# Kernel tuning notes

Hardware: AMD Instinct MI355X
Metric: run time of the kernel (lower is better)

The kernel has to match this reference:

```python
import jax, jax.numpy as jnp
import numpy as np

B, T, F, H = 256, 1024, 64, 128
DT = 1.0
EPS = 1e-5


def _layer_norm(h, g, b):
    mu = jnp.mean(h, axis=-1, keepdims=True)
    var = jnp.var(h, axis=-1, keepdims=True)
    return (h - mu) * jax.lax.rsqrt(var + EPS) * g + b


def setup_inputs() -> dict:
    key = jax.random.key(0)
    ks = jax.random.split(key, 8)
    def xavier(k, shape):
        fan_in, fan_out = shape[1], shape[0]
        lim = np.sqrt(6.0 / (fan_in + fan_out))
        return jax.random.uniform(k, shape, jnp.float32, -lim, lim)
    return {
        "x": jax.random.normal(ks[0], (B, T, F), jnp.float32),
        # layer 0 (input_dim=F)
        "Wh0": xavier(ks[1], (H, H)), "bh0": jnp.zeros((H,), jnp.float32),
        "Wx0": xavier(ks[2], (H, F)), "bx0": jnp.zeros((H,), jnp.float32),
        "Wt0": xavier(ks[3], (H, F)), "bt0": jnp.zeros((H,), jnp.float32),
        "tau0": jnp.ones((H,), jnp.float32),
        "g0": jnp.ones((H,), jnp.float32), "be0": jnp.zeros((H,), jnp.float32),
        # layer 1 (input_dim=H)
        "Wh1": xavier(ks[4], (H, H)), "bh1": jnp.zeros((H,), jnp.float32),
        "Wx1": xavier(ks[5], (H, H)), "bx1": jnp.zeros((H,), jnp.float32),
        "Wt1": xavier(ks[6], (H, H)), "bt1": jnp.zeros((H,), jnp.float32),
        "tau1": jnp.ones((H,), jnp.float32),
        "g1": jnp.ones((H,), jnp.float32), "be1": jnp.zeros((H,), jnp.float32),
    }


def _cell(x_t, h, Wh, bh, Wx, bx, Wt, bt, tau_base):
    f = jnp.tanh(h @ Wh.T + bh + x_t @ Wx.T + bx)        # (B,H)
    tau = tau_base + jax.nn.softplus(x_t @ Wt.T + bt)     # (B,H)
    return h + (DT / tau) * (-h + f)


def reference(x, Wh0, bh0, Wx0, bx0, Wt0, bt0, tau0, g0, be0,
              Wh1, bh1, Wx1, bx1, Wt1, bt1, tau1, g1, be1):
    xT = jnp.transpose(x, (1, 0, 2))  # (T,B,F)

    def step(carry, x_t):
        h0, h1 = carry
        h0 = _layer_norm(_cell(x_t, h0, Wh0, bh0, Wx0, bx0, Wt0, bt0, tau0), g0, be0)
        h1 = _layer_norm(_cell(h0, h1, Wh1, bh1, Wx1, bx1, Wt1, bt1, tau1), g1, be1)
        return (h0, h1), None

    h_init = (jnp.zeros((x.shape[0], H), x.dtype), jnp.zeros((x.shape[0], H), x.dtype))
    (h0, h1), _ = jax.lax.scan(step, h_init, xT)
    return h1  # hidden_dim == latent_dim, no proj
```

## Files before the change

kernel.cpp:

```cpp
#include <hip/hip_runtime.h>
#include <stdint.h>


#define B_ 256
#define T_ 1024
#define F_ 64
#define H_ 128
#define EPS_ 1e-5f
#define NT_ 512

typedef _Float16 h2 __attribute__((ext_vector_type(2)));
typedef _Float16 h8 __attribute__((ext_vector_type(8)));
typedef float f32x4 __attribute__((ext_vector_type(4)));
typedef __fp16  f16v2 __attribute__((ext_vector_type(2)));

__device__ __forceinline__ h2 pkf16(float a, float b) {
  union { f16v2 f; h2 h; } c;
  c.f = __builtin_amdgcn_cvt_pkrtz(a, b);
  return c.h;
}
__device__ __forceinline__ uint32_t as_u32(h2 h) { union { h2 h; uint32_t u; } c; c.h = h; return c.u; }

#if __has_builtin(__builtin_amdgcn_rsqf)
__device__ __forceinline__ float rsq_fast(float x) { return __builtin_amdgcn_rsqf(x); }
#else
__device__ __forceinline__ float rsq_fast(float x) { return rsqrtf(x); }
#endif

#if __has_builtin(__builtin_amdgcn_update_dpp)
template <int CTRL>
__device__ __forceinline__ float dpp_add(float v) {
  union { float f; int i; } a, b;
  a.f = v;
  b.i = __builtin_amdgcn_update_dpp(0, a.i, CTRL, 0xf, 0xf, true);
  return v + b.f;
}
__device__ __forceinline__ float red16(float v) {
  v = dpp_add<0x128>(v);
  v = dpp_add<0x124>(v);
  v = dpp_add<0x122>(v);
  v = dpp_add<0x121>(v);
  return v;
}
#else
__device__ __forceinline__ float red16(float v) {
  v += __shfl_xor(v, 1); v += __shfl_xor(v, 2);
  v += __shfl_xor(v, 4); v += __shfl_xor(v, 8);
  return v;
}
#endif

__device__ __forceinline__ h8 packfrag(const float* p) {
  float4 a = *(const float4*)p;
  float4 b = *(const float4*)(p + 4);
  union { h2 h[4]; h8 v; } c;
  c.h[0] = pkf16(a.x, a.y); c.h[1] = pkf16(a.z, a.w);
  c.h[2] = pkf16(b.x, b.y); c.h[3] = pkf16(b.z, b.w);
  return c.v;
}
__device__ __forceinline__ h8 packfrag_g(const float* w, const float* gv, const float* bv,
                                         float& dg, float& dbe) {
  float4 a = *(const float4*)w;
  float4 b = *(const float4*)(w + 4);
  float4 ga = *(const float4*)gv;
  float4 gb = *(const float4*)(gv + 4);
  float4 ba = *(const float4*)bv;
  float4 bb = *(const float4*)(bv + 4);
  float w0 = a.x*ga.x, w1 = a.y*ga.y, w2 = a.z*ga.z, w3 = a.w*ga.w;
  float w4 = b.x*gb.x, w5 = b.y*gb.y, w6 = b.z*gb.z, w7 = b.w*gb.w;
  dg  += (w0 + w1) + (w2 + w3) + (w4 + w5) + (w6 + w7);
  dbe += a.x*ba.x + a.y*ba.y + a.z*ba.z + a.w*ba.w
       + b.x*bb.x + b.y*bb.y + b.z*bb.z + b.w*bb.w;
  union { h2 h[4]; h8 v; } c;
  c.h[0] = pkf16(w0, w1); c.h[1] = pkf16(w2, w3);
  c.h[2] = pkf16(w4, w5); c.h[3] = pkf16(w6, w7);
  return c.v;
}
__device__ __forceinline__ h8 ldfrag(const uint32_t* p) {
  union { uint4 u; h8 v; } c;
  c.u = *(const uint4*)p;
  return c.v;
}

__device__ __forceinline__ float tanh_fast(float a) {
  float aa = fabsf(a);
  float e  = __expf(2.f * aa);
  float th = 1.f - 2.f * __builtin_amdgcn_rcpf(e + 1.f);
  return copysignf(th, a);
}
__device__ __forceinline__ float softplus_fast(float x) {
  return (x > 20.f) ? x : __logf(1.f + __expf(x));
}

#define MFMA16(A_, B_, C_) __builtin_amdgcn_mfma_f32_16x16x32_f16(A_, B_, C_, 0, 0, 0)

__global__ void __attribute__((amdgpu_flat_work_group_size(NT_, NT_)))
                __attribute__((amdgpu_waves_per_eu(2, 2)))
ltc_scan(
    const float* __restrict__ x,
    const float* __restrict__ Wh0, const float* __restrict__ bh0,
    const float* __restrict__ Wx0, const float* __restrict__ bx0,
    const float* __restrict__ Wt0, const float* __restrict__ bt0,
    const float* __restrict__ tau0, const float* __restrict__ g0,
    const float* __restrict__ be0,
    const float* __restrict__ Wh1, const float* __restrict__ bh1,
    const float* __restrict__ Wx1, const float* __restrict__ bx1,
    const float* __restrict__ Wt1, const float* __restrict__ bt1,
    const float* __restrict__ tau1, const float* __restrict__ g1,
    const float* __restrict__ be1,
    float* __restrict__ out)
{
  __shared__ __align__(16) uint32_t h0p[2][64];
  __shared__ __align__(16) uint32_t h1p[2][64];
  __shared__ __align__(16) uint32_t x4[4][32];
  __shared__ __align__(16) float    part[4][4];

  const int tid = threadIdx.x;
  const int wid = tid >> 6;
  const int l   = tid & 63;
  const int g4  = (l >> 4) << 2;
  const int g8  = (l >> 4) << 3;
  const int b   = blockIdx.x;
  const float* xg = x + (size_t)b * (T_ * F_);
  const bool selT1 = (l & 16) != 0;

  if (tid < 128) { ((uint32_t*)h0p)[tid] = 0u; ((uint32_t*)h1p)[tid] = 0u; }
  if (tid < 16)  ((float*)part)[tid] = 0.f;
  if (tid < 32) {
    float2 a = *(const float2*)(xg + 2 * tid);
    float2 c = *(const float2*)(xg + F_ + 2 * tid);
    x4[0][tid] = as_u32(pkf16(a.x, a.y));
    x4[1][tid] = as_u32(pkf16(c.x, c.y));
  }
  __syncthreads();

  if (wid < 4) {
    const int c0 = wid * 32 + (l & 15);
    const int ct = wid * 32 + (l & 31);
    h8 wh0[4], wh1[4], wx0[2], wx1[2], wt0[2], wt1[2];
    float cg, cb;
    {
      float dg0 = 0.f, db0 = 0.f, dg1 = 0.f, db1 = 0.f;
      const float* p0 = Wh0 + c0 * H_ + g8;
      const float* p1 = Wh0 + (c0 + 16) * H_ + g8;
      #pragma unroll
      for (int m = 0; m < 4; ++m) {
        wh0[m] = packfrag_g(p0 + 32 * m, g0 + g8 + 32 * m, be0 + g8 + 32 * m, dg0, db0);
        wh1[m] = packfrag_g(p1 + 32 * m, g0 + g8 + 32 * m, be0 + g8 + 32 * m, dg1, db1);
      }
      dg0 += __shfl_xor(dg0, 16); dg0 += __shfl_xor(dg0, 32);
      db0 += __shfl_xor(db0, 16); db0 += __shfl_xor(db0, 32);
      dg1 += __shfl_xor(dg1, 16); dg1 += __shfl_xor(dg1, 32);
      db1 += __shfl_xor(db1, 16); db1 += __shfl_xor(db1, 32);
      cg = selT1 ? dg1 : dg0; cb = selT1 ? db1 : db0;
      const float* q0 = Wx0 + c0 * F_ + g8;
      const float* q1 = Wx0 + (c0 + 16) * F_ + g8;
      const float* r0 = Wt0 + c0 * F_ + g8;
      const float* r1 = Wt0 + (c0 + 16) * F_ + g8;
      #pragma unroll
      for (int m = 0; m < 2; ++m) {
        wx0[m] = packfrag(q0 + 32 * m); wx1[m] = packfrag(q1 + 32 * m);
        wt0[m] = packfrag(r0 + 32 * m); wt1[m] = packfrag(r1 + 32 * m);
      }
    }
    const float bhx = bh0[ct] + bx0[ct];
    const float btr = bt0[ct], taub = tau0[ct], gr = g0[ct], ber = be0[ct];
    const int  widx = wid * 16 + ((l & 31) >> 1);
    const bool wlane = ((l & 33) == 0);
    const bool st = (wid == 0) && (l < 32);

    float hcp = 0.f;
    float2 xcur;
    if (st) xcur = *(const float2*)(xg + 2 * F_ + 2 * l);

    #pragma unroll 4
    for (int i = 0; i <= T_; ++i) {
      const float2 stt = *(const float2*)&part[(i + 3) & 3][0];
      if (st) {
        x4[(i + 2) & 3][l] = as_u32(pkf16(xcur.x, xcur.y));
        int tn = (i + 3 < T_) ? (i + 3) : (T_ - 1);
        xcur = *(const float2*)(xg + tn * F_ + 2 * l);
      }
      const uint32_t* ub = h0p[(i + 1) & 1];
      const uint32_t* xb = x4[i & 3];
      f32x4 aH0 = {0.f,0.f,0.f,0.f}, aH1 = {0.f,0.f,0.f,0.f};
      f32x4 aX0 = {0.f,0.f,0.f,0.f}, aX1 = {0.f,0.f,0.f,0.f};
      f32x4 aT0 = {0.f,0.f,0.f,0.f}, aT1 = {0.f,0.f,0.f,0.f};
      #pragma unroll
      for (int m = 0; m < 4; ++m) {
        h8 af = ldfrag(ub + m * 16 + g4);
        aH0 = MFMA16(af, wh0[m], aH0);
        aH1 = MFMA16(af, wh1[m], aH1);
      }
      #pragma unroll
      for (int m = 0; m < 2; ++m) {
        h8 xf = ldfrag(xb + m * 16 + g4);
        aX0 = MFMA16(xf, wx0[m], aX0);
        aX1 = MFMA16(xf, wx1[m], aX1);
        aT0 = MFMA16(xf, wt0[m], aT0);
        aT1 = MFMA16(xf, wt1[m], aT1);
      }
      float aH = selT1 ? aH1[0] : aH0[0];
      float aX = selT1 ? aX1[0] : aX0[0];
      float aT = selT1 ? aT1[0] : aT0[0];
      float mu = stt.x * (1.f / 128.f);
      float m2 = stt.y * (1.f / 128.f);
      float rstd = rsq_fast(m2 - mu * mu + EPS_);
      float fl = (i > 0) ? 1.f : 0.f;
      float sc = fl * rstd;
      float pa = fmaf(sc, aH, fmaf(-sc * mu, cg, fl * cb)) + aX + bhx;
      float pt = aT + btr;
      float f   = tanh_fast(pa);
      float tau = taub + softplus_fast(pt);
      float hold = fl * fmaf((hcp - mu) * rstd, gr, ber);
      float hc  = fmaf(f - hold, __builtin_amdgcn_rcpf(tau), hold);
      float hc2 = __shfl_xor(hc, 1);
      if (wlane) h0p[i & 1][widx] = as_u32(pkf16(hc, hc2));
      float v = (l & 32) ? hc * hc : hc;
      v = red16(v); v += __shfl_xor(v, 16);
      if (l == 0)  atomicAdd(&part[i & 3][0], v);
      if (l == 32) atomicAdd(&part[i & 3][1], v);
      hcp = hc;
      __syncthreads();
    }
  } else {
    const int c0 = (wid - 4) * 32 + (l & 15);
    const int ct = (wid - 4) * 32 + (l & 31);
    h8 vh0[4], vh1[4], vx0[4], vx1[4], vt0[4], vt1[4];
    float cAg, cAb, cBg, cBb, cTg, cTb;
    {
      float d1=0.f,d2=0.f,d3=0.f,d4=0.f,d5=0.f,d6=0.f;
      float e1=0.f,e2=0.f,e3=0.f,e4=0.f,e5=0.f,e6=0.f;
      const float* p0 = Wh1 + c0 * H_ + g8;
      const float* p1 = Wh1 + (c0 + 16) * H_ + g8;
      const float* q0 = Wx1 + c0 * H_ + g8;
      const float* q1 = Wx1 + (c0 + 16) * H_ + g8;
      const float* r0 = Wt1 + c0 * H_ + g8;
      const float* r1 = Wt1 + (c0 + 16) * H_ + g8;
      #pragma unroll
      for (int m = 0; m < 4; ++m) {
        vh0[m] = packfrag_g(p0 + 32 * m, g1 + g8 + 32 * m, be1 + g8 + 32 * m, d1, d2);
        vh1[m] = packfrag_g(p1 + 32 * m, g1 + g8 + 32 * m, be1 + g8 + 32 * m, e1, e2);
        vx0[m] = packfrag_g(q0 + 32 * m, g0 + g8 + 32 * m, be0 + g8 + 32 * m, d3, d4);
        vx1[m] = packfrag_g(q1 + 32 * m, g0 + g8 + 32 * m, be0 + g8 + 32 * m, e3, e4);
        vt0[m] = packfrag_g(r0 + 32 * m, g0 + g8 + 32 * m, be0 + g8 + 32 * m, d5, d6);
        vt1[m] = packfrag_g(r1 + 32 * m, g0 + g8 + 32 * m, be0 + g8 + 32 * m, e5, e6);
      }
      d1 += __shfl_xor(d1, 16); d1 += __shfl_xor(d1, 32);
      d2 += __shfl_xor(d2, 16); d2 += __shfl_xor(d2, 32);
      d3 += __shfl_xor(d3, 16); d3 += __shfl_xor(d3, 32);
      d4 += __shfl_xor(d4, 16); d4 += __shfl_xor(d4, 32);
      d5 += __shfl_xor(d5, 16); d5 += __shfl_xor(d5, 32);
      d6 += __shfl_xor(d6, 16); d6 += __shfl_xor(d6, 32);
      e1 += __shfl_xor(e1, 16); e1 += __shfl_xor(e1, 32);
      e2 += __shfl_xor(e2, 16); e2 += __shfl_xor(e2, 32);
      e3 += __shfl_xor(e3, 16); e3 += __shfl_xor(e3, 32);
      e4 += __shfl_xor(e4, 16); e4 += __shfl_xor(e4, 32);
      e5 += __shfl_xor(e5, 16); e5 += __shfl_xor(e5, 32);
      e6 += __shfl_xor(e6, 16); e6 += __shfl_xor(e6, 32);
      cAg = selT1 ? e1 : d1; cAb = selT1 ? e2 : d2;
      cBg = selT1 ? e3 : d3; cBb = selT1 ? e4 : d4;
      cTg = selT1 ? e5 : d5; cTb = selT1 ? e6 : d6;
    }
    const float bhx = bh1[ct] + bx1[ct];
    const float btr = bt1[ct], taub = tau1[ct], gr = g1[ct], ber = be1[ct];
    const int  widx = (wid - 4) * 16 + ((l & 31) >> 1);
    const bool wlane = ((l & 33) == 0);
    const bool zt = (tid == NT_ - 1);

    float hcp = 0.f;
    #pragma unroll 2
    for (int i = 0; i <= T_; ++i) {
      const float4 P = *(const float4*)&part[(i + 3) & 3][0];
      if (zt) *(float4*)&part[(i + 2) & 3][0] = make_float4(0.f, 0.f, 0.f, 0.f);
      const uint32_t* u1b = h1p[(i + 1) & 1];
      const uint32_t* u0b = h0p[(i + 1) & 1];
      f32x4 aA0 = {0.f,0.f,0.f,0.f}, aA1 = {0.f,0.f,0.f,0.f};
      f32x4 aB0 = {0.f,0.f,0.f,0.f}, aB1 = {0.f,0.f,0.f,0.f};
      f32x4 aT0 = {0.f,0.f,0.f,0.f}, aT1 = {0.f,0.f,0.f,0.f};
      #pragma unroll
      for (int m = 0; m < 4; ++m) {
        h8 af = ldfrag(u1b + m * 16 + g4);
        aA0 = MFMA16(af, vh0[m], aA0);
        aA1 = MFMA16(af, vh1[m], aA1);
      }
      #pragma unroll
      for (int m = 0; m < 4; ++m) {
        h8 f0 = ldfrag(u0b + m * 16 + g4);
        aB0 = MFMA16(f0, vx0[m], aB0);
        aB1 = MFMA16(f0, vx1[m], aB1);
        aT0 = MFMA16(f0, vt0[m], aT0);
        aT1 = MFMA16(f0, vt1[m], aT1);
      }
      float aA = selT1 ? aA1[0] : aA0[0];
      float aB = selT1 ? aB1[0] : aB0[0];
      float aT = selT1 ? aT1[0] : aT0[0];
      float mu0 = P.x * (1.f / 128.f), m20 = P.y * (1.f / 128.f);
      float mu1 = P.z * (1.f / 128.f), m21 = P.w * (1.f / 128.f);
      float rstd0 = rsq_fast(m20 - mu0 * mu0 + EPS_);
      float rstd1 = rsq_fast(m21 - mu1 * mu1 + EPS_);
      float fl0 = (i > 0) ? 1.f : 0.f;
      float fl1 = (i > 1) ? 1.f : 0.f;
      float sc0 = fl0 * rstd0, sc1 = fl1 * rstd1;
      float pa = fmaf(sc1, aA, fmaf(-sc1 * mu1, cAg, fl1 * cAb))
               + fmaf(sc0, aB, fmaf(-sc0 * mu0, cBg, fl0 * cBb)) + bhx;
      float pt = fmaf(sc0, aT, fmaf(-sc0 * mu0, cTg, fl0 * cTb)) + btr;
      float f   = tanh_fast(pa);
      float tau = taub + softplus_fast(pt);
      float hold = fl1 * fmaf((hcp - mu1) * rstd1, gr, ber);
      float hc  = fmaf(f - hold, __builtin_amdgcn_rcpf(tau), hold);
      float hc2 = __shfl_xor(hc, 1);
      bool we = (i > 0);
      if (we && wlane) h1p[i & 1][widx] = as_u32(pkf16(hc, hc2));
      float v = (l & 32) ? hc * hc : hc;
      v = red16(v); v += __shfl_xor(v, 16);
      if (we && l == 0)  atomicAdd(&part[i & 3][2], v);
      if (we && l == 32) atomicAdd(&part[i & 3][3], v);
      if (we) hcp = hc;
      __syncthreads();
    }
    {
      float mu1 = part[T_ & 3][2] * (1.f / 128.f);
      float m21 = part[T_ & 3][3] * (1.f / 128.f);
      float rstd1 = rsq_fast(m21 - mu1 * mu1 + EPS_);
      float hn = fmaf((hcp - mu1) * rstd1, gr, ber);
      if (l < 32) out[b * H_ + ct] = hn;
    }
  }
}

extern "C" void kernel_launch(void* const* d_in, const int* in_sizes, int n_in,
                              void* d_out, int out_size, void* d_ws, size_t ws_size,
                              hipStream_t stream) {
  const float* x    = (const float*)d_in[0];
  const float* Wh0  = (const float*)d_in[1];
  const float* bh0  = (const float*)d_in[2];
  const float* Wx0  = (const float*)d_in[3];
  const float* bx0  = (const float*)d_in[4];
  const float* Wt0  = (const float*)d_in[5];
  const float* bt0  = (const float*)d_in[6];
  const float* tau0 = (const float*)d_in[7];
  const float* g0   = (const float*)d_in[8];
  const float* be0  = (const float*)d_in[9];
  const float* Wh1  = (const float*)d_in[10];
  const float* bh1  = (const float*)d_in[11];
  const float* Wx1  = (const float*)d_in[12];
  const float* bx1  = (const float*)d_in[13];
  const float* Wt1  = (const float*)d_in[14];
  const float* bt1  = (const float*)d_in[15];
  const float* tau1 = (const float*)d_in[16];
  const float* g1   = (const float*)d_in[17];
  const float* be1  = (const float*)d_in[18];
  float* out        = (float*)d_out;

  ltc_scan<<<B_, NT_, 0, stream>>>(x, Wh0, bh0, Wx0, bx0, Wt0, bt0, tau0, g0, be0,
                                   Wh1, bh1, Wx1, bx1, Wt1, bt1, tau1, g1, be1, out);
}
```

Before: 1.015 ms.

## Pack two batch rows per 1024-thread block to halve block count

Each block now handles two independent batch rows with 16 waves, using per-row shared buffers and statistics slots, and the grid is halved. The aim is to raise per-CU occupancy and overlap two independent recurrences so each one's latency is hidden. The cost is that only half as many blocks run, both rows share one barrier per step, and the tighter waves-per-EU bound cuts the register budget, which may force weight fragments to spill.

```diff
diff --git a/kernel.cpp b/kernel.cpp
--- a/kernel.cpp
+++ b/kernel.cpp
@@ -7,7 +7,7 @@
 #define F_ 64
 #define H_ 128
 #define EPS_ 1e-5f
-#define NT_ 512
+#define NT_ 1024
 
 typedef _Float16 h2 __attribute__((ext_vector_type(2)));
 typedef _Float16 h8 __attribute__((ext_vector_type(8)));
@@ -95,7 +95,7 @@
 #define MFMA16(A_, B_, C_) __builtin_amdgcn_mfma_f32_16x16x32_f16(A_, B_, C_, 0, 0, 0)
 
 __global__ void __attribute__((amdgpu_flat_work_group_size(NT_, NT_)))
-                __attribute__((amdgpu_waves_per_eu(2, 2)))
+                __attribute__((amdgpu_waves_per_eu(4, 4)))
 ltc_scan(
     const float* __restrict__ x,
     const float* __restrict__ Wh0, const float* __restrict__ bh0,
@@ -110,33 +110,35 @@
     const float* __restrict__ be1,
     float* __restrict__ out)
 {
-  __shared__ __align__(16) uint32_t h0p[2][64];
-  __shared__ __align__(16) uint32_t h1p[2][64];
-  __shared__ __align__(16) uint32_t x4[4][32];
-  __shared__ __align__(16) float    part[4][4];
+  __shared__ __align__(16) uint32_t h0p[2][2][64];
+  __shared__ __align__(16) uint32_t h1p[2][2][64];
+  __shared__ __align__(16) uint32_t x4[2][4][32];
+  __shared__ __align__(16) float    part[2][4][4];
 
   const int tid = threadIdx.x;
   const int wid = tid >> 6;
+  const int r   = wid >> 3;
+  const int w8  = wid & 7;
   const int l   = tid & 63;
   const int g4  = (l >> 4) << 2;
   const int g8  = (l >> 4) << 3;
-  const int b   = blockIdx.x;
-  const float* xg = x + (size_t)b * (T_ * F_);
+  const int row = blockIdx.x * 2 + r;
+  const float* xg = x + (size_t)row * (T_ * F_);
   const bool selT1 = (l & 16) != 0;
 
-  if (tid < 128) { ((uint32_t*)h0p)[tid] = 0u; ((uint32_t*)h1p)[tid] = 0u; }
-  if (tid < 16)  ((float*)part)[tid] = 0.f;
-  if (tid < 32) {
-    float2 a = *(const float2*)(xg + 2 * tid);
-    float2 c = *(const float2*)(xg + F_ + 2 * tid);
-    x4[0][tid] = as_u32(pkf16(a.x, a.y));
-    x4[1][tid] = as_u32(pkf16(c.x, c.y));
+  if (tid < 256) { ((uint32_t*)h0p)[tid] = 0u; ((uint32_t*)h1p)[tid] = 0u; }
+  if (tid < 32)  ((float*)part)[tid] = 0.f;
+  if (w8 == 0 && l < 32) {
+    float2 a = *(const float2*)(xg + 2 * l);
+    float2 c = *(const float2*)(xg + F_ + 2 * l);
+    x4[r][0][l] = as_u32(pkf16(a.x, a.y));
+    x4[r][1][l] = as_u32(pkf16(c.x, c.y));
   }
   __syncthreads();
 
-  if (wid < 4) {
-    const int c0 = wid * 32 + (l & 15);
-    const int ct = wid * 32 + (l & 31);
+  if (w8 < 4) {
+    const int c0 = w8 * 32 + (l & 15);
+    const int ct = w8 * 32 + (l & 31);
     h8 wh0[4], wh1[4], wx0[2], wx1[2], wt0[2], wt1[2];
     float cg, cb;
     {
@@ -165,9 +167,9 @@
     }
     const float bhx = bh0[ct] + bx0[ct];
     const float btr = bt0[ct], taub = tau0[ct], gr = g0[ct], ber = be0[ct];
-    const int  widx = wid * 16 + ((l & 31) >> 1);
+    const int  widx = w8 * 16 + ((l & 31) >> 1);
     const bool wlane = ((l & 33) == 0);
-    const bool st = (wid == 0) && (l < 32);
+    const bool st = (w8 == 0) && (l < 32);
 
     float hcp = 0.f;
     float2 xcur;
@@ -175,14 +177,14 @@
 
     #pragma unroll 4
     for (int i = 0; i <= T_; ++i) {
-      const float2 stt = *(const float2*)&part[(i + 3) & 3][0];
+      const float2 stt = *(const float2*)&part[r][(i + 3) & 3][0];
       if (st) {
-        x4[(i + 2) & 3][l] = as_u32(pkf16(xcur.x, xcur.y));
+        x4[r][(i + 2) & 3][l] = as_u32(pkf16(xcur.x, xcur.y));
         int tn = (i + 3 < T_) ? (i + 3) : (T_ - 1);
         xcur = *(const float2*)(xg + tn * F_ + 2 * l);
       }
-      const uint32_t* ub = h0p[(i + 1) & 1];
-      const uint32_t* xb = x4[i & 3];
+      const uint32_t* ub = h0p[r][(i + 1) & 1];
+      const uint32_t* xb = x4[r][i & 3];
       f32x4 aH0 = {0.f,0.f,0.f,0.f}, aH1 = {0.f,0.f,0.f,0.f};
       f32x4 aX0 = {0.f,0.f,0.f,0.f}, aX1 = {0.f,0.f,0.f,0.f};
       f32x4 aT0 = {0.f,0.f,0.f,0.f}, aT1 = {0.f,0.f,0.f,0.f};
@@ -215,17 +217,17 @@
       float hold = fl * fmaf((hcp - mu) * rstd, gr, ber);
       float hc  = fmaf(f - hold, __builtin_amdgcn_rcpf(tau), hold);
       float hc2 = __shfl_xor(hc, 1);
-      if (wlane) h0p[i & 1][widx] = as_u32(pkf16(hc, hc2));
+      if (wlane) h0p[r][i & 1][widx] = as_u32(pkf16(hc, hc2));
       float v = (l & 32) ? hc * hc : hc;
       v = red16(v); v += __shfl_xor(v, 16);
-      if (l == 0)  atomicAdd(&part[i & 3][0], v);
-      if (l == 32) atomicAdd(&part[i & 3][1], v);
+      if (l == 0)  atomicAdd(&part[r][i & 3][0], v);
+      if (l == 32) atomicAdd(&part[r][i & 3][1], v);
       hcp = hc;
       __syncthreads();
     }
   } else {
-    const int c0 = (wid - 4) * 32 + (l & 15);
-    const int ct = (wid - 4) * 32 + (l & 31);
+    const int c0 = (w8 - 4) * 32 + (l & 15);
+    const int ct = (w8 - 4) * 32 + (l & 31);
     h8 vh0[4], vh1[4], vx0[4], vx1[4], vt0[4], vt1[4];
     float cAg, cAb, cBg, cBb, cTg, cTb;
     {
@@ -264,17 +266,17 @@
     }
     const float bhx = bh1[ct] + bx1[ct];
     const float btr = bt1[ct], taub = tau1[ct], gr = g1[ct], ber = be1[ct];
-    const int  widx = (wid - 4) * 16 + ((l & 31) >> 1);
+    const int  widx = (w8 - 4) * 16 + ((l & 31) >> 1);
     const bool wlane = ((l & 33) == 0);
-    const bool zt = (tid == NT_ - 1);
+    const bool zt = (w8 == 7 && l == 63);
 
     float hcp = 0.f;
     #pragma unroll 2
     for (int i = 0; i <= T_; ++i) {
-      const float4 P = *(const float4*)&part[(i + 3) & 3][0];
-      if (zt) *(float4*)&part[(i + 2) & 3][0] = make_float4(0.f, 0.f, 0.f, 0.f);
-      const uint32_t* u1b = h1p[(i + 1) & 1];
-      const uint32_t* u0b = h0p[(i + 1) & 1];
+      const float4 P = *(const float4*)&part[r][(i + 3) & 3][0];
+      if (zt) *(float4*)&part[r][(i + 2) & 3][0] = make_float4(0.f, 0.f, 0.f, 0.f);
+      const uint32_t* u1b = h1p[r][(i + 1) & 1];
+      const uint32_t* u0b = h0p[r][(i + 1) & 1];
       f32x4 aA0 = {0.f,0.f,0.f,0.f}, aA1 = {0.f,0.f,0.f,0.f};
       f32x4 aB0 = {0.f,0.f,0.f,0.f}, aB1 = {0.f,0.f,0.f,0.f};
       f32x4 aT0 = {0.f,0.f,0.f,0.f}, aT1 = {0.f,0.f,0.f,0.f};
@@ -311,20 +313,20 @@
       float hc  = fmaf(f - hold, __builtin_amdgcn_rcpf(tau), hold);
       float hc2 = __shfl_xor(hc, 1);
       bool we = (i > 0);
-      if (we && wlane) h1p[i & 1][widx] = as_u32(pkf16(hc, hc2));
+      if (we && wlane) h1p[r][i & 1][widx] = as_u32(pkf16(hc, hc2));
       float v = (l & 32) ? hc * hc : hc;
       v = red16(v); v += __shfl_xor(v, 16);
-      if (we && l == 0)  atomicAdd(&part[i & 3][2], v);
-      if (we && l == 32) atomicAdd(&part[i & 3][3], v);
+      if (we && l == 0)  atomicAdd(&part[r][i & 3][2], v);
+      if (we && l == 32) atomicAdd(&part[r][i & 3][3], v);
       if (we) hcp = hc;
       __syncthreads();
     }
     {
-      float mu1 = part[T_ & 3][2] * (1.f / 128.f);
-      float m21 = part[T_ & 3][3] * (1.f / 128.f);
+      float mu1 = part[r][T_ & 3][2] * (1.f / 128.f);
+      float m21 = part[r][T_ & 3][3] * (1.f / 128.f);
       float rstd1 = rsq_fast(m21 - mu1 * mu1 + EPS_);
       float hn = fmaf((hcp - mu1) * rstd1, gr, ber);
-      if (l < 32) out[b * H_ + ct] = hn;
+      if (l < 32) out[row * H_ + ct] = hn;
     }
   }
 }
@@ -353,6 +355,6 @@
   const float* be1  = (const float*)d_in[18];
   float* out        = (float*)d_out;
 
-  ltc_scan<<<B_, NT_, 0, stream>>>(x, Wh0, bh0, Wx0, bx0, Wt0, bt0, tau0, g0, be0,
-                                   Wh1, bh1, Wx1, bx1, Wt1, bt1, tau1, g1, be1, out);
-}
+  ltc_scan<<<B_ / 2, NT_, 0, stream>>>(x, Wh0, bh0, Wx0, bx0, Wt0, bt0, tau0, g0, be0,
+                                       Wh1, bh1, Wx1, bx1, Wt1, bt1, tau1, g1, be1, out);
+}
```

Measured after the change: 2.730 ms. 2.69x slower.

## Replace per-step block barriers with LDS flag-based producer/consumer sync between layer waves

Applied to the files above, without the earlier changes.

Replaces the __syncthreads at every timestep with per-wave done counters in shared memory that are polled with s_sleep. Layer-0 waves can now run up to three steps ahead of layer-1 waves through 4-deep ring buffers for hidden states and partial sums. The LDS atomicAdd reductions become per-wave partial-sum slots that consumers add up, and the layer-1 loop is re-indexed so its one-step skew no longer needs an extra iteration. The intent is to decouple the two layers and remove lock-step barrier stalls. The cost is spin-wait polling overhead and reliance on volatile LDS ordering being correct.

```diff
diff --git a/kernel.cpp b/kernel.cpp
--- a/kernel.cpp
+++ b/kernel.cpp
@@ -49,6 +49,17 @@
   return v;
 }
 #endif
+
+__device__ __forceinline__ void wait4(volatile int* a, int tgt) {
+  if (tgt <= 0) return;
+  for (;;) {
+    int m0 = a[0], m1 = a[1], m2 = a[2], m3 = a[3];
+    int m = min(min(m0, m1), min(m2, m3));
+    if (m >= tgt) break;
+    __builtin_amdgcn_s_sleep(1);
+  }
+  __threadfence_block();
+}
 
 __device__ __forceinline__ h8 packfrag(const float* p) {
   float4 a = *(const float4*)p;
@@ -110,10 +121,13 @@
     const float* __restrict__ be1,
     float* __restrict__ out)
 {
-  __shared__ __align__(16) uint32_t h0p[2][64];
-  __shared__ __align__(16) uint32_t h1p[2][64];
-  __shared__ __align__(16) uint32_t x4[4][32];
-  __shared__ __align__(16) float    part[4][4];
+  __shared__ __align__(16) uint32_t h0p[4][64];
+  __shared__ __align__(16) uint32_t h1p[4][64];
+  __shared__ __align__(16) uint32_t x4r[4][32];
+  __shared__ __align__(16) float2   p0s[4][4];
+  __shared__ __align__(16) float2   p1s[4][4];
+  __shared__ volatile int done0[4];
+  __shared__ volatile int done1[4];
 
   const int tid = threadIdx.x;
   const int wid = tid >> 6;
@@ -124,13 +138,14 @@
   const float* xg = x + (size_t)b * (T_ * F_);
   const bool selT1 = (l & 16) != 0;
 
-  if (tid < 128) { ((uint32_t*)h0p)[tid] = 0u; ((uint32_t*)h1p)[tid] = 0u; }
-  if (tid < 16)  ((float*)part)[tid] = 0.f;
+  if (tid < 256) { ((uint32_t*)h0p)[tid] = 0u; ((uint32_t*)h1p)[tid] = 0u; }
+  if (tid < 32)  { ((float*)p0s)[tid] = 0.f; ((float*)p1s)[tid] = 0.f; }
+  if (tid < 4)   { done0[tid] = 0; done1[tid] = 0; }
   if (tid < 32) {
     float2 a = *(const float2*)(xg + 2 * tid);
     float2 c = *(const float2*)(xg + F_ + 2 * tid);
-    x4[0][tid] = as_u32(pkf16(a.x, a.y));
-    x4[1][tid] = as_u32(pkf16(c.x, c.y));
+    x4r[0][tid] = as_u32(pkf16(a.x, a.y));
+    x4r[1][tid] = as_u32(pkf16(c.x, c.y));
   }
   __syncthreads();
 
@@ -173,16 +188,21 @@
     float2 xcur;
     if (st) xcur = *(const float2*)(xg + 2 * F_ + 2 * l);
 
-    #pragma unroll 4
-    for (int i = 0; i <= T_; ++i) {
-      const float2 stt = *(const float2*)&part[(i + 3) & 3][0];
+    for (int i = 0; i < T_; ++i) {
+      wait4(done0, i);
+      wait4(done1, i - 3);
+      const float4* sp = (const float4*)&p0s[(i + 3) & 3][0];
+      float ss, s2s;
+      { float4 sa = sp[0], sb = sp[1];
+        ss  = (sa.x + sa.z) + (sb.x + sb.z);
+        s2s = (sa.y + sa.w) + (sb.y + sb.w); }
       if (st) {
-        x4[(i + 2) & 3][l] = as_u32(pkf16(xcur.x, xcur.y));
+        x4r[(i + 2) & 3][l] = as_u32(pkf16(xcur.x, xcur.y));
         int tn = (i + 3 < T_) ? (i + 3) : (T_ - 1);
         xcur = *(const float2*)(xg + tn * F_ + 2 * l);
       }
-      const uint32_t* ub = h0p[(i + 1) & 1];
-      const uint32_t* xb = x4[i & 3];
+      const uint32_t* ub = h0p[(i + 3) & 3];
+      const uint32_t* xb = x4r[i & 3];
       f32x4 aH0 = {0.f,0.f,0.f,0.f}, aH1 = {0.f,0.f,0.f,0.f};
       f32x4 aX0 = {0.f,0.f,0.f,0.f}, aX1 = {0.f,0.f,0.f,0.f};
       f32x4 aT0 = {0.f,0.f,0.f,0.f}, aT1 = {0.f,0.f,0.f,0.f};
@@ -203,8 +223,8 @@
       float aH = selT1 ? aH1[0] : aH0[0];
       float aX = selT1 ? aX1[0] : aX0[0];
       float aT = selT1 ? aT1[0] : aT0[0];
-      float mu = stt.x * (1.f / 128.f);
-      float m2 = stt.y * (1.f / 128.f);
+      float mu = ss * (1.f / 128.f);
+      float m2 = s2s * (1.f / 128.f);
       float rstd = rsq_fast(m2 - mu * mu + EPS_);
       float fl = (i > 0) ? 1.f : 0.f;
       float sc = fl * rstd;
@@ -215,13 +235,14 @@
       float hold = fl * fmaf((hcp - mu) * rstd, gr, ber);
       float hc  = fmaf(f - hold, __builtin_amdgcn_rcpf(tau), hold);
       float hc2 = __shfl_xor(hc, 1);
-      if (wlane) h0p[i & 1][widx] = as_u32(pkf16(hc, hc2));
+      if (wlane) h0p[i & 3][widx] = as_u32(pkf16(hc, hc2));
       float v = (l & 32) ? hc * hc : hc;
       v = red16(v); v += __shfl_xor(v, 16);
-      if (l == 0)  atomicAdd(&part[i & 3][0], v);
-      if (l == 32) atomicAdd(&part[i & 3][1], v);
+      float v2 = __shfl_down(v, 32);
+      if (l == 0) p0s[i & 3][wid] = make_float2(v, v2);
       hcp = hc;
-      __syncthreads();
+      __threadfence_block();
+      if (l == 0) done0[wid] = i + 1;
     }
   } else {
     const int c0 = (wid - 4) * 32 + (l & 15);
@@ -266,15 +287,23 @@
     const float btr = bt1[ct], taub = tau1[ct], gr = g1[ct], ber = be1[ct];
     const int  widx = (wid - 4) * 16 + ((l & 31) >> 1);
     const bool wlane = ((l & 33) == 0);
-    const bool zt = (tid == NT_ - 1);
+    const int  bw = wid - 4;
 
     float hcp = 0.f;
-    #pragma unroll 2
-    for (int i = 0; i <= T_; ++i) {
-      const float4 P = *(const float4*)&part[(i + 3) & 3][0];
-      if (zt) *(float4*)&part[(i + 2) & 3][0] = make_float4(0.f, 0.f, 0.f, 0.f);
-      const uint32_t* u1b = h1p[(i + 1) & 1];
-      const uint32_t* u0b = h0p[(i + 1) & 1];
+    for (int j = 0; j < T_; ++j) {
+      wait4(done0, j + 1);
+      wait4(done1, j);
+      float ss0, s20, ss1, s21;
+      { const float4* sp = (const float4*)&p0s[j & 3][0];
+        float4 sa = sp[0], sb = sp[1];
+        ss0 = (sa.x + sa.z) + (sb.x + sb.z);
+        s20 = (sa.y + sa.w) + (sb.y + sb.w); }
+      { const float4* sp = (const float4*)&p1s[(j + 3) & 3][0];
+        float4 sa = sp[0], sb = sp[1];
+        ss1 = (sa.x + sa.z) + (sb.x + sb.z);
+        s21 = (sa.y + sa.w) + (sb.y + sb.w); }
+      const uint32_t* u1b = h1p[(j + 3) & 3];
+      const uint32_t* u0b = h0p[j & 3];
       f32x4 aA0 = {0.f,0.f,0.f,0.f}, aA1 = {0.f,0.f,0.f,0.f};
       f32x4 aB0 = {0.f,0.f,0.f,0.f}, aB1 = {0.f,0.f,0.f,0.f};
       f32x4 aT0 = {0.f,0.f,0.f,0.f}, aT1 = {0.f,0.f,0.f,0.f};
@@ -295,33 +324,38 @@
       float aA = selT1 ? aA1[0] : aA0[0];
       float aB = selT1 ? aB1[0] : aB0[0];
       float aT = selT1 ? aT1[0] : aT0[0];
-      float mu0 = P.x * (1.f / 128.f), m20 = P.y * (1.f / 128.f);
-      float mu1 = P.z * (1.f / 128.f), m21 = P.w * (1.f / 128.f);
+      float mu0 = ss0 * (1.f / 128.f), m20 = s20 * (1.f / 128.f);
+      float mu1 = ss1 * (1.f / 128.f), m21 = s21 * (1.f / 128.f);
       float rstd0 = rsq_fast(m20 - mu0 * mu0 + EPS_);
       float rstd1 = rsq_fast(m21 - mu1 * mu1 + EPS_);
-      float fl0 = (i > 0) ? 1.f : 0.f;
-      float fl1 = (i > 1) ? 1.f : 0.f;
-      float sc0 = fl0 * rstd0, sc1 = fl1 * rstd1;
+      float fl1 = (j > 0) ? 1.f : 0.f;
+      float sc1 = fl1 * rstd1;
       float pa = fmaf(sc1, aA, fmaf(-sc1 * mu1, cAg, fl1 * cAb))
-               + fmaf(sc0, aB, fmaf(-sc0 * mu0, cBg, fl0 * cBb)) + bhx;
-      float pt = fmaf(sc0, aT, fmaf(-sc0 * mu0, cTg, fl0 * cTb)) + btr;
+               + fmaf(rstd0, aB, fmaf(-rstd0 * mu0, cBg, cBb)) + bhx;
+      float pt = fmaf(rstd0, aT, fmaf(-rstd0 * mu0, cTg, cTb)) + btr;
       float f   = tanh_fast(pa);
       float tau = taub + softplus_fast(pt);
       float hold = fl1 * fmaf((hcp - mu1) * rstd1, gr, ber);
       float hc  = fmaf(f - hold, __builtin_amdgcn_rcpf(tau), hold);
       float hc2 = __shfl_xor(hc, 1);
-      bool we = (i > 0);
-      if (we && wlane) h1p[i & 1][widx] = as_u32(pkf16(hc, hc2));
+      if (wlane) h1p[j & 3][widx] = as_u32(pkf16(hc, hc2));
       float v = (l & 32) ? hc * hc : hc;
       v = red16(v); v += __shfl_xor(v, 16);
-      if (we && l == 0)  atomicAdd(&part[i & 3][2], v);
-      if (we && l == 32) atomicAdd(&part[i & 3][3], v);
-      if (we) hcp = hc;
-      __syncthreads();
-    }
+      float v2 = __shfl_down(v, 32);
+      if (l == 0) p1s[j & 3][bw] = make_float2(v, v2);
+      hcp = hc;
+      __threadfence_block();
+      if (l == 0) done1[bw] = j + 1;
+    }
+    wait4(done1, T_);
     {
-      float mu1 = part[T_ & 3][2] * (1.f / 128.f);
-      float m21 = part[T_ & 3][3] * (1.f / 128.f);
+      float ss1, s21;
+      { const float4* sp = (const float4*)&p1s[(T_ - 1) & 3][0];
+        float4 sa = sp[0], sb = sp[1];
+        ss1 = (sa.x + sa.z) + (sb.x + sb.z);
+        s21 = (sa.y + sa.w) + (sb.y + sb.w); }
+      float mu1 = ss1 * (1.f / 128.f);
+      float m21 = s21 * (1.f / 128.f);
       float rstd1 = rsq_fast(m21 - mu1 * mu1 + EPS_);
       float hn = fmaf((hcp - mu1) * rstd1, gr, ber);
       if (l < 32) out[b * H_ + ct] = hn;
```

Result: slower. 1.216 ms (+19.8%).
